# Kernel optimization log

Hardware: AMD Instinct MI355X
Metric: run time of the kernel (lower is better)

The kernel has to match this reference:

```python
import jax, jax.numpy as jnp
import numpy as np
from jax import lax

NEG = -1e30  # log-space -inf surrogate

def setup_inputs() -> dict:
    key = jax.random.key(0)
    ks = jax.random.split(key, 6)
    B, T, D, V, Lmax = 16, 800, 512, 4000, 100
    hs_pad = jax.random.normal(ks[0], (B, T, D), dtype=jnp.float32)
    W = jax.random.normal(ks[1], (D, V), dtype=jnp.float32) * 0.02
    b = jnp.zeros((V,), dtype=jnp.float32)
    hlens = jax.random.randint(ks[2], (B,), 400, T + 1, dtype=jnp.int32)
    ys_pad = jax.random.randint(ks[3], (B, Lmax), 1, V, dtype=jnp.int32)
    ys_lens = jax.random.randint(ks[4], (B,), 50, Lmax + 1, dtype=jnp.int32)
    return {"hs_pad": hs_pad, "W": W, "b": b, "hlens": hlens,
            "ys_pad": ys_pad, "ys_lens": ys_lens}

def _ctc_loss(lp, ys_pad, hlens, ys_lens):
    # lp: [T, B, V] log-probs; blank = 0
    T, B, V = lp.shape
    Lmax = ys_pad.shape[1]
    S = 2 * Lmax + 1  # extended label length: blank-interleaved
    ext = jnp.zeros((B, S), dtype=ys_pad.dtype).at[:, 1::2].set(ys_pad)
    # skip transition s-2 -> s allowed when ext[s] != blank and ext[s] != ext[s-2]
    skip = jnp.concatenate(
        [jnp.zeros((B, 2), dtype=bool),
         (ext[:, 2:] != 0) & (ext[:, 2:] != ext[:, :-2])], axis=1)
    # per-frame emission log-probs for extended labels: [T, B, S]
    emit = jnp.take_along_axis(lp, jnp.broadcast_to(ext[None], (T, B, S)), axis=2)
    alpha0 = jnp.full((B, S), NEG, dtype=lp.dtype).at[:, :2].set(emit[0, :, :2])

    def step(alpha, inp):
        emit_t, active = inp  # [B, S], [B]
        s1 = jnp.pad(alpha[:, :-1], ((0, 0), (1, 0)), constant_values=NEG)
        s2 = jnp.pad(alpha[:, :-2], ((0, 0), (2, 0)), constant_values=NEG)
        s2 = jnp.where(skip, s2, NEG)
        new = jnp.logaddexp(jnp.logaddexp(alpha, s1), s2) + emit_t
        alpha = jnp.where(active[:, None], new, alpha)  # freeze past hlen
        return alpha, None

    active = jnp.arange(1, T)[:, None] < hlens[None, :]  # [T-1, B]
    alpha, _ = lax.scan(step, alpha0, (emit[1:], active))
    idx = (2 * ys_lens).astype(jnp.int32)  # last blank position
    a_last = jnp.take_along_axis(alpha, idx[:, None], axis=1)[:, 0]
    a_prev = jnp.take_along_axis(alpha, (idx - 1)[:, None], axis=1)[:, 0]
    loss = -jnp.logaddexp(a_last, a_prev)
    # zero_infinity=True
    return jnp.where(jnp.isfinite(loss) & (loss < 1e29), loss, 0.0)

def reference(hs_pad, W, b, hlens, ys_pad, ys_lens):
    # ctc_lo projection (dropout_rate=0.0) -> [T, B, V] -> log_softmax
    logits = jnp.einsum('btd,dv->btv', hs_pad, W) + b
    lp = jax.nn.log_softmax(logits, axis=-1).transpose(1, 0, 2)
    loss = _ctc_loss(lp, ys_pad, hlens, ys_lens)
    B = hs_pad.shape[0]
    return loss.sum() / B  # reduce=True: sum / batch size
```

## Files before the change

kernel.cpp:

```cpp
#include <hip/hip_runtime.h>
#include <hip/hip_bf16.h>
#include <math.h>

#define NEGV -1e30f
#define LN2F 0.6931471805599453f


typedef __attribute__((ext_vector_type(8))) short bf16x8;
typedef __attribute__((ext_vector_type(4))) float f32x4;

__device__ __forceinline__ short f2bf(float x) {
    __hip_bfloat16 h = __float2bfloat16(x);
    return __builtin_bit_cast(short, h);
}

__device__ __forceinline__ float shup1(float x) {
    return __builtin_bit_cast(float,
        __builtin_amdgcn_update_dpp(0, __builtin_bit_cast(int, x),
                                    0x138, 0xf, 0xf, true));
}

#define GLD_LDS(g, l) \
    __builtin_amdgcn_global_load_lds( \
        (const __attribute__((address_space(1))) void*)(g), \
        (__attribute__((address_space(3))) void*)(l), 16, 0, 0)

#define LOADX4(dst, addr, off) \
    asm volatile("global_load_dwordx4 %0, %1, off offset:" #off \
                 : "=&v"(dst) : "v"(addr) : "memory")

#define WAITV(n) do { \
    asm volatile("s_waitcnt vmcnt(" #n ")" ::: "memory"); \
    __builtin_amdgcn_sched_barrier(0); \
} while (0)

#define ISSUE_SET(pa, pb, it, af, bfr) do { \
    const short* _a = (pa) + (size_t)(it) * 4096; \
    const short* _b = (pb) + (size_t)(it) * 4096; \
    LOADX4(af[0], _a, 0);    LOADX4(af[1], _a, 1024); \
    LOADX4(af[2], _a, 2048); LOADX4(af[3], _a, 3072); \
    LOADX4(bfr[0], _b, 0);    LOADX4(bfr[1], _b, 1024); \
    LOADX4(bfr[2], _b, 2048); LOADX4(bfr[3], _b, 3072); \
} while (0)

__global__ __launch_bounds__(256) void prep(
    const float* __restrict__ hs, const float* __restrict__ W,
    const float* __restrict__ bias, const int* __restrict__ ys,
    short* __restrict__ W2, short* __restrict__ A2,
    float* __restrict__ biasp, unsigned char* __restrict__ M,
    unsigned char* __restrict__ canon, float* __restrict__ lse_sum,
    float* __restrict__ out)
{
    __shared__ float tile[32][65];
    __shared__ unsigned char mapl[4096];
    const int bx = blockIdx.x, tid = threadIdx.x;

    if (bx < 1024) {
        const int n0 = (bx & 63) * 64;
        const int k0 = (bx >> 6) * 32;
        #pragma unroll
        for (int p = 0; p < 8; p++) {
            int idx = p * 256 + tid;
            int k = idx >> 6, n = idx & 63;
            int gn = n0 + n;
            tile[k][n] = (gn < 4000) ? W[(size_t)(k0 + k) * 4000 + gn] : 0.0f;
        }
        __syncthreads();
        const int nn = tid >> 6, lane = tid & 63;
        const int l16 = lane & 15, quad = lane >> 4;
        const int ct = n0 >> 7, wn = (n0 >> 6) & 1, it = k0 >> 5;
        size_t chunk = ((((size_t)ct * 16 + it) * 2 + wn) * 4 + nn) * 64 + lane;
        bf16x8 r;
        #pragma unroll
        for (int j = 0; j < 8; j++) r[j] = f2bf(tile[quad * 8 + j][nn * 16 + l16]);
        *(bf16x8*)(W2 + chunk * 8) = r;
    } else if (bx < 4224) {
        int g = (bx - 1024) * 256 + tid;
        int lane = g & 63, mi = (g >> 6) & 3, wm = (g >> 8) & 1;
        int it = (g >> 9) & 15, rb = g >> 13;
        int row = rb * 128 + wm * 64 + mi * 16 + (lane & 15);
        int k = it * 32 + (lane >> 4) * 8;
        const float* src = hs + (size_t)row * 512 + k;
        float4 u = *(const float4*)src;
        float4 v = *(const float4*)(src + 4);
        bf16x8 r;
        r[0] = f2bf(u.x); r[1] = f2bf(u.y); r[2] = f2bf(u.z); r[3] = f2bf(u.w);
        r[4] = f2bf(v.x); r[5] = f2bf(v.y); r[6] = f2bf(v.z); r[7] = f2bf(v.w);
        *(bf16x8*)(A2 + (size_t)g * 8) = r;
    } else {
        for (int b = 0; b < 16; b++) {
            for (int i = tid; i < 1024; i += 256)
                ((unsigned int*)mapl)[i] = 0xFFFFFFFFu;
            __syncthreads();
            if (tid == 0) mapl[0] = 0;
            __syncthreads();
            if (tid < 100) mapl[ys[b * 100 + tid]] = (unsigned char)(tid + 1);
            __syncthreads();
            for (int i = tid; i < 1024; i += 256)
                ((unsigned int*)(M + (size_t)b * 4096))[i] = ((const unsigned int*)mapl)[i];
            if (tid < 128) {
                int colc = (tid >= 1 && tid <= 100) ? ys[b * 100 + tid - 1] : 0;
                canon[b * 128 + tid] = mapl[colc];
            }
            __syncthreads();
        }
        for (int i = tid; i < 4096; i += 256)
            biasp[i] = (i < 4000) ? bias[i] : NEGV;
        for (int i = tid; i < 12800; i += 256)
            lse_sum[i] = 0.0f;
        if (tid == 0) out[0] = 0.0f;
    }
}

__device__ __forceinline__ void mfma_cluster(
    const bf16x8 af[4], const bf16x8 bfr[4], f32x4 acc[4][4])
{
    #pragma unroll
    for (int mi = 0; mi < 4; mi++)
        #pragma unroll
        for (int ni = 0; ni < 4; ni++)
            acc[mi][ni] = __builtin_amdgcn_mfma_f32_16x16x32_bf16(
                af[mi], bfr[ni], acc[mi][ni], 0, 0, 0);
}

__global__ __launch_bounds__(256) void lse_mfma(
    const short* __restrict__ A2,
    const short* __restrict__ W2,
    const float* __restrict__ biasp,
    const unsigned char* __restrict__ M,
    float* __restrict__ lse_sum,
    __hip_bfloat16* __restrict__ Praw)
{
    const unsigned int bid = blockIdx.x;
    const unsigned int xcd = bid & 7;
    const unsigned int s = bid >> 3;
    const unsigned int ct = s / 13;
    const unsigned int rl = s - ct * 13;
    const unsigned int rt = rl * 8 + xcd;
    if (rt >= 100) return;

    const int tid = threadIdx.x;
    const int w = tid >> 6, lane = tid & 63;
    const int quad = lane >> 4, l16 = lane & 15;
    const int wm = w >> 1, wn = w & 1;
    const int row0 = rt * 128;
    const int col0 = ct * 128;

    const short* Abase = A2 + ((size_t)rt * 32 + wm) * 2048 + lane * 8;
    const short* Bbase = W2 + ((size_t)ct * 32 + wn) * 2048 + lane * 8;

    f32x4 acc[4][4];
    #pragma unroll
    for (int mi = 0; mi < 4; mi++)
        #pragma unroll
        for (int ni = 0; ni < 4; ni++) acc[mi][ni] = (f32x4){0.f,0.f,0.f,0.f};

    bf16x8 fa[4][4], fb[4][4];
    ISSUE_SET(Abase, Bbase, 0, fa[0], fb[0]);
    ISSUE_SET(Abase, Bbase, 1, fa[1], fb[1]);
    ISSUE_SET(Abase, Bbase, 2, fa[2], fb[2]);
    ISSUE_SET(Abase, Bbase, 3, fa[3], fb[3]);

    #pragma unroll
    for (int p = 0; p < 16; p++) {
        if (p < 13)      { WAITV(24); }
        else if (p == 13){ WAITV(16); }
        else if (p == 14){ WAITV(8);  }
        else             { WAITV(0);  }
        __builtin_amdgcn_s_setprio(1);
        mfma_cluster(fa[p & 3], fb[p & 3], acc);
        __builtin_amdgcn_s_setprio(0);
        if (p < 12) ISSUE_SET(Abase, Bbase, p + 4, fa[p & 3], fb[p & 3]);
    }
    __builtin_amdgcn_sched_barrier(0);

    const int b0i = row0 / 800;
    const int b1i = (b0i + 1 < 16) ? b0i + 1 : 15;
    const int bbound = (b0i + 1) * 800;
    float sv[16];
    #pragma unroll
    for (int i = 0; i < 16; i++) sv[i] = 0.0f;
    #pragma unroll
    for (int ni = 0; ni < 4; ni++) {
        int col = col0 + wn * 64 + ni * 16 + l16;
        float bj = biasp[col];
        unsigned char sl0 = M[(size_t)b0i * 4096 + col];
        unsigned char sl1 = M[(size_t)b1i * 4096 + col];
        #pragma unroll
        for (int mi = 0; mi < 4; mi++) {
            #pragma unroll
            for (int r = 0; r < 4; r++) {
                int row = row0 + wm * 64 + mi * 16 + quad * 4 + r;
                float v = acc[mi][ni][r] + bj;
                sv[mi * 4 + r] += __expf(v);
                unsigned char sl = (row < bbound) ? sl0 : sl1;
                if (sl != 255)
                    Praw[(size_t)row * 128 + sl] = __float2bfloat16(v);
            }
        }
    }
    #pragma unroll
    for (int off = 1; off < 16; off <<= 1)
        #pragma unroll
        for (int i = 0; i < 16; i++) sv[i] += __shfl_xor(sv[i], off);
    if (l16 == 0) {
        #pragma unroll
        for (int mi = 0; mi < 4; mi++)
            #pragma unroll
            for (int r = 0; r < 4; r++)
                atomicAdd(&lse_sum[row0 + wm * 64 + mi * 16 + quad * 4 + r],
                          sv[mi * 4 + r]);
    }
}

__global__ __launch_bounds__(256) void pexp(
    const __hip_bfloat16* __restrict__ Praw,
    const float* __restrict__ lse_sum,
    const unsigned char* __restrict__ canon,
    float* __restrict__ PE)
{
    __shared__ unsigned char st[224];
    __shared__ float scs[16];
    const int bp = blockIdx.x;
    const int b = bp / 50, rr = bp - b * 50;
    const int tid = threadIdx.x;
    const unsigned char* cb = canon + b * 128;
    if (tid < 224) {
        int idx = (tid + 1) >> 1;
        st[tid] = (tid & 1) ? cb[idx < 128 ? idx : 127] : (unsigned char)0;
    }
    const int row0 = b * 800 + rr * 16;
    if (tid < 16) scs[tid] = __builtin_amdgcn_rcpf(lse_sum[row0 + tid]) * 2048.0f;
    __syncthreads();
    for (int item = tid; item < 832; item += 256) {
        int i = item / 52, sg = item - i * 52;
        int row = row0 + i;
        const __hip_bfloat16* pr = Praw + (size_t)row * 128;
        float sc = scs[i];
        int s0 = sg * 4;
        float4 o;
        o.x = (s0 + 0 <= 200) ? __expf(__bfloat162float(pr[st[s0 + 0]])) * sc : 0.f;
        o.y = (s0 + 1 <= 200) ? __expf(__bfloat162float(pr[st[s0 + 1]])) * sc : 0.f;
        o.z = (s0 + 2 <= 200) ? __expf(__bfloat162float(pr[st[s0 + 2]])) * sc : 0.f;
        o.w = (s0 + 3 <= 200) ? __expf(__bfloat162float(pr[st[s0 + 3]])) * sc : 0.f;
        *(float4*)&PE[(size_t)row * 208 + s0] = o;
    }
}

__global__ __launch_bounds__(256) void ctc_dp(
    const float* __restrict__ PE,
    const int* __restrict__ hlens,
    const int* __restrict__ ys,
    const int* __restrict__ ylens,
    float* __restrict__ out)
{
    const int b = blockIdx.x, tid = threadIdx.x;
    const int w = tid >> 6, lane = tid & 63;
    __shared__ float emS[2][13376];
    __shared__ float sA[256];

    const float* Pb = PE + (size_t)b * 800 * 208;
    const int hl = hlens[b], L = ylens[b];
    const int t_stop = hl - 1;
    const int C = (t_stop + 63) >> 6;

    const int yb = b * 100;
    float kA = 0.f, kB = 0.f, kH = 0.f;
    if (lane >= 1 && 2 * lane <= 99)
        kA = (ys[yb + 2 * lane] != ys[yb + 2 * lane - 1]) ? 1.f : 0.f;
    if (2 * lane + 1 <= 99)
        kB = (ys[yb + 2 * lane + 1] != ys[yb + 2 * lane]) ? 1.f : 0.f;
    if (lane >= 1 && 2 * lane - 1 <= 99)
        kH = (ys[yb + 2 * lane - 1] != ys[yb + 2 * lane - 2]) ? 1.f : 0.f;
    const float m0  = (lane <= 50) ? 1.f : 0.f;
    const float m13 = (lane <= 49) ? 1.f : 0.f;

    float a0 = 0.f, a1 = 0.f, a2 = 0.f, a3 = 0.f;
    if (w == 0 && lane == 0) {
        a0 = Pb[0];
        a1 = Pb[1];
    }
    int kacc = 0;

    {
        const char* src = (const char*)(Pb + 208);
        char* dst = (char*)&emS[0][0];
        #pragma unroll
        for (int j = 0; j < 13; j++) {
            int idx = tid + 256 * j;
            GLD_LDS(src + (size_t)idx * 16, dst + (size_t)idx * 16);
        }
    }
    __syncthreads();

    for (int ch = 0; ch < C; ch++) {
        if (w > 0) {
            int nc = ch + 1;
            if (nc < C) {
                const char* src = (const char*)(Pb + (size_t)(64 * nc + 1) * 208);
                char* dst = (char*)&emS[nc & 1][0];
                const int base = tid - 64;
                #pragma unroll
                for (int j = 0; j < 18; j++) {
                    int idx = base + 192 * j;
                    if (idx < 3328)
                        GLD_LDS(src + (size_t)idx * 16, dst + (size_t)idx * 16);
                }
            }
        } else {
            const float* bb = emS[ch & 1];
            const int t0 = 64 * ch + 1;
            const int soff = 4 * lane;
            if (t0 + 63 <= t_stop) {
                f32x4 e = *(const f32x4*)&bb[0 * 208 + soff];
                f32x4 f = *(const f32x4*)&bb[1 * 208 + soff];
                #pragma unroll
                for (int k = 0; k < 32; k++) {
                    f32x4 en = (f32x4){0.f,0.f,0.f,0.f};
                    f32x4 fn = (f32x4){0.f,0.f,0.f,0.f};
                    if (k < 31) {
                        en = *(const f32x4*)&bb[(2 * k + 2) * 208 + soff];
                        fn = *(const f32x4*)&bb[(2 * k + 3) * 208 + soff];
                    }
                    float pht = shup1(e[3]);
                    float h1 = shup1(a3);
                    float h2 = shup1(a2);
                    float h3 = shup1(a1);
                    float tm1 = fmaf(kH, h3, h1 + h2);
                    float t0v = a0 + h1;
                    float t1v = fmaf(kA, h1, a1 + a0);
                    float t2v = a2 + a1;
                    float t3v = fmaf(kB, a1, a3 + a2);
                    float um1 = pht * tm1;
                    float u0 = e[0] * t0v, u1 = e[1] * t1v;
                    float u2 = e[2] * t2v, u3 = e[3] * t3v;
                    a0 = (f[0] * (u0 + um1)) * m0;
                    a1 = (f[1] * fmaf(kA, um1, u1 + u0)) * m13;
                    a2 = (f[2] * (u2 + u1)) * m13;
                    a3 = (f[3] * fmaf(kB, u1, u3 + u2)) * m13;
                    if ((k & 7) == 7) {
                        int tc = t0 + 2 * k + 1;
                        float lm = fmaxf(fmaxf(a0, a1), fmaxf(a2, a3));
                        int sa1 = (2 * L < tc) ? 2 * L : tc;
                        int sa2 = (int)(2.0f * L * tc / hl);
                        float v1 = __shfl(lm, sa1 >> 2);
                        float v2 = __shfl(lm, sa2 >> 2);
                        float av = fmaxf(v1, v2);
                        int eb = (__float_as_int(av) >> 23) & 0xFF;
                        if (eb != 0 && eb != 255) {
                            int e2i = eb - 127;
                            kacc += e2i;
                            float sc = __int_as_float((127 - e2i) << 23);
                            a0 *= sc; a1 *= sc; a2 *= sc; a3 *= sc;
                        }
                    }
                    e = en; f = fn;
                }
            } else {
                for (int t = t0; t <= t_stop; t++) {
                    if ((t & 15) == 0) {
                        float lm = fmaxf(fmaxf(a0, a1), fmaxf(a2, a3));
                        int sa1 = (2 * L < t) ? 2 * L : t;
                        int sa2 = (int)(2.0f * L * t / hl);
                        float v1 = __shfl(lm, sa1 >> 2);
                        float v2 = __shfl(lm, sa2 >> 2);
                        float av = fmaxf(v1, v2);
                        int eb = (__float_as_int(av) >> 23) & 0xFF;
                        if (eb != 0 && eb != 255) {
                            int e2i = eb - 127;
                            kacc += e2i;
                            float sc = __int_as_float((127 - e2i) << 23);
                            a0 *= sc; a1 *= sc; a2 *= sc; a3 *= sc;
                        }
                    }
                    f32x4 e = *(const f32x4*)&bb[(t - t0) * 208 + soff];
                    float p3 = shup1(a3);
                    float n0 = (a0 + p3) * e[0];
                    float n1 = fmaf(kA, p3, a1 + a0) * e[1];
                    float n2 = (a2 + a1) * e[2];
                    float n3 = fmaf(kB, a1, a3 + a2) * e[3];
                    a0 = n0 * m0; a1 = n1 * m13; a2 = n2 * m13; a3 = n3 * m13;
                }
            }
        }
        __syncthreads();
    }

    if (w == 0) {
        sA[lane * 4 + 0] = a0; sA[lane * 4 + 1] = a1;
        sA[lane * 4 + 2] = a2; sA[lane * 4 + 3] = a3;
    }
    __syncthreads();

    if (tid == 0) {
        int idx = 2 * L;
        float s = sA[idx] + sA[idx - 1];
        float la = __logf(s) + (float)(kacc - 11 * hl) * LN2F;
        float loss = -la;
        if (!isfinite(loss) || loss >= 1e29f) loss = 0.0f;
        atomicAdd(out, loss * 0.0625f);
    }
}

extern "C" void kernel_launch(void* const* d_in, const int* in_sizes, int n_in,
                              void* d_out, int out_size, void* d_ws, size_t ws_size,
                              hipStream_t stream)
{
    const float* hs    = (const float*)d_in[0];
    const float* W     = (const float*)d_in[1];
    const float* bias  = (const float*)d_in[2];
    const int*   hlens = (const int*)d_in[3];
    const int*   ys    = (const int*)d_in[4];
    const int*   ylens = (const int*)d_in[5];
    float* out = (float*)d_out;

    char* wsb = (char*)d_ws;
    short* W2      = (short*)(wsb);
    short* A2      = (short*)(wsb + 4194304);
    float* PE      = (float*)(wsb + 4194304);
    float* biasp   = (float*)(wsb + 17301504);
    __hip_bfloat16* Praw = (__hip_bfloat16*)(wsb + 17317888);
    float* lse_sum = (float*)(wsb + 20594688);
    unsigned char* M     = (unsigned char*)(wsb + 20645888);
    unsigned char* canon = (unsigned char*)(wsb + 20711424);

    hipLaunchKernelGGL(prep,     dim3(4225), dim3(256), 0, stream,
                       hs, W, bias, ys, W2, A2, biasp, M, canon, lse_sum, out);
    hipLaunchKernelGGL(lse_mfma, dim3(3328), dim3(256), 0, stream,
                       A2, W2, biasp, M, lse_sum, Praw);
    hipLaunchKernelGGL(pexp,     dim3(800),  dim3(256), 0, stream,
                       Praw, lse_sum, canon, PE);
    hipLaunchKernelGGL(ctc_dp,   dim3(16),   dim3(256), 0, stream,
                       PE, hlens, ys, ylens, out);
}
```

Before: 224.5 us.

## Stage GEMM operands through triple-buffered LDS with direct global-to-LDS loads

Replaces per-wave direct global-to-register dwordx4 loads, where each wave fetched its own A and B fragments, with a cooperative triple-buffered LDS pipeline. Each wave copies part of the tile using global_load_lds, and a block barrier runs every K step. This removes duplicate global fetches of the shared A and B tiles across waves, in exchange for LDS reads, extra barriers and 48KB of shared memory that may reduce occupancy.

```diff
diff --git a/kernel.cpp b/kernel.cpp
--- a/kernel.cpp
+++ b/kernel.cpp
@@ -25,22 +25,9 @@
         (const __attribute__((address_space(1))) void*)(g), \
         (__attribute__((address_space(3))) void*)(l), 16, 0, 0)
 
-#define LOADX4(dst, addr, off) \
-    asm volatile("global_load_dwordx4 %0, %1, off offset:" #off \
-                 : "=&v"(dst) : "v"(addr) : "memory")
-
 #define WAITV(n) do { \
     asm volatile("s_waitcnt vmcnt(" #n ")" ::: "memory"); \
     __builtin_amdgcn_sched_barrier(0); \
-} while (0)
-
-#define ISSUE_SET(pa, pb, it, af, bfr) do { \
-    const short* _a = (pa) + (size_t)(it) * 4096; \
-    const short* _b = (pb) + (size_t)(it) * 4096; \
-    LOADX4(af[0], _a, 0);    LOADX4(af[1], _a, 1024); \
-    LOADX4(af[2], _a, 2048); LOADX4(af[3], _a, 3072); \
-    LOADX4(bfr[0], _b, 0);    LOADX4(bfr[1], _b, 1024); \
-    LOADX4(bfr[2], _b, 2048); LOADX4(bfr[3], _b, 3072); \
 } while (0)
 
 __global__ __launch_bounds__(256) void prep(
@@ -146,8 +133,21 @@
     const int row0 = rt * 128;
     const int col0 = ct * 128;
 
-    const short* Abase = A2 + ((size_t)rt * 32 + wm) * 2048 + lane * 8;
-    const short* Bbase = W2 + ((size_t)ct * 32 + wn) * 2048 + lane * 8;
+    __shared__ __align__(16) short sbuf[3][8192];
+
+    const short* gsrc = ((w < 2) ? (A2 + (size_t)rt * 65536)
+                                 : (W2 + (size_t)ct * 65536))
+                        + (w & 1) * 2048 + lane * 8;
+    const int lds_off = ((w < 2) ? 0 : 4096) + (w & 1) * 2048 + lane * 8;
+
+#define STAGE(s_, bi_) do { \
+    const short* _g = gsrc + (size_t)(s_) * 4096; \
+    short* _l = &sbuf[bi_][lds_off]; \
+    GLD_LDS(_g,        _l); \
+    GLD_LDS(_g + 512,  _l + 512); \
+    GLD_LDS(_g + 1024, _l + 1024); \
+    GLD_LDS(_g + 1536, _l + 1536); \
+} while (0)
 
     f32x4 acc[4][4];
     #pragma unroll
@@ -155,23 +155,37 @@
         #pragma unroll
         for (int ni = 0; ni < 4; ni++) acc[mi][ni] = (f32x4){0.f,0.f,0.f,0.f};
 
-    bf16x8 fa[4][4], fb[4][4];
-    ISSUE_SET(Abase, Bbase, 0, fa[0], fb[0]);
-    ISSUE_SET(Abase, Bbase, 1, fa[1], fb[1]);
-    ISSUE_SET(Abase, Bbase, 2, fa[2], fb[2]);
-    ISSUE_SET(Abase, Bbase, 3, fa[3], fb[3]);
-
-    #pragma unroll
-    for (int p = 0; p < 16; p++) {
-        if (p < 13)      { WAITV(24); }
-        else if (p == 13){ WAITV(16); }
-        else if (p == 14){ WAITV(8);  }
-        else             { WAITV(0);  }
+    STAGE(0, 0);
+    STAGE(1, 1);
+    WAITV(4);
+    __builtin_amdgcn_s_barrier();
+    __builtin_amdgcn_sched_barrier(0);
+
+    #pragma unroll
+    for (int it = 0; it < 16; ++it) {
+        if (it + 2 < 16) STAGE(it + 2, (it + 2) % 3);
+
+        const short* cb = &sbuf[it % 3][0];
+        const short* ap = cb + wm * 2048 + lane * 8;
+        const short* bp = cb + 4096 + wn * 2048 + lane * 8;
+        bf16x8 af[4], bfr[4];
+        #pragma unroll
+        for (int mi = 0; mi < 4; mi++) af[mi]  = *(const bf16x8*)(ap + mi * 512);
+        #pragma unroll
+        for (int ni = 0; ni < 4; ni++) bfr[ni] = *(const bf16x8*)(bp + ni * 512);
+
         __builtin_amdgcn_s_setprio(1);
-        mfma_cluster(fa[p & 3], fb[p & 3], acc);
+        mfma_cluster(af, bfr, acc);
         __builtin_amdgcn_s_setprio(0);
-        if (p < 12) ISSUE_SET(Abase, Bbase, p + 4, fa[p & 3], fb[p & 3]);
-    }
+
+        if (it < 15) {
+            if (it < 14) { WAITV(4); }
+            else         { WAITV(0); }
+            __builtin_amdgcn_s_barrier();
+            __builtin_amdgcn_sched_barrier(0);
+        }
+    }
+#undef STAGE
     __builtin_amdgcn_sched_barrier(0);
 
     const int b0i = row0 / 800;
```

Result: no change. 227.8 us (+1.5%).
